# Performance work log

Measured on AMD Instinct MI355X. Metric: run time of the kernel, lower is better.

## Reference

```python
import jax, jax.numpy as jnp
import numpy as np

B, N_SRC, N_TGT = 2, 2048, 2048
DIM, HEADS, DIM_HEAD, DIM_ROT = 1024, 16, 64, 32
INNER = HEADS * DIM_HEAD
SCALE = DIM_HEAD ** -0.5


def rotate_every_two(x):
    # (..., d) with d even: pairs (x1, x2) -> (-x2, x1), interleaved
    x1 = x[..., ::2]
    x2 = x[..., 1::2]
    return jnp.stack((-x2, x1), axis=-1).reshape(x.shape)


def setup_inputs() -> dict:
    key = jax.random.key(0)
    ks = jax.random.split(key, 10)
    return {
        "src": jax.random.normal(ks[0], (B, N_SRC, DIM), jnp.float32),
        "sin_src": jax.random.uniform(ks[1], (B, N_SRC, DIM_ROT), jnp.float32, -1.0, 1.0),
        "cos_src": jax.random.uniform(ks[2], (B, N_SRC, DIM_ROT), jnp.float32, -1.0, 1.0),
        "tgt": jax.random.normal(ks[3], (B, N_TGT, DIM), jnp.float32),
        "sin_tgt": jax.random.uniform(ks[4], (B, N_TGT, DIM_ROT), jnp.float32, -1.0, 1.0),
        "cos_tgt": jax.random.uniform(ks[5], (B, N_TGT, DIM_ROT), jnp.float32, -1.0, 1.0),
        "wq": jax.random.normal(ks[6], (DIM, INNER), jnp.float32) / np.sqrt(DIM),
        "wkv": jax.random.normal(ks[7], (DIM, 2 * INNER), jnp.float32) / np.sqrt(DIM),
        "wout": jax.random.normal(ks[8], (INNER, DIM), jnp.float32) / np.sqrt(INNER),
        "bout": jnp.zeros((DIM,), jnp.float32),
    }


def reference(src, sin_src, cos_src, tgt, sin_tgt, cos_tgt, wq, wkv, wout, bout):
    b = src.shape[0]
    q = tgt @ wq                                  # (b, i, inner)
    k, v = jnp.split(src @ wkv, 2, axis=-1)       # (b, j, inner) each

    def split_heads(t):
        return t.reshape(b, t.shape[1], HEADS, DIM_HEAD).transpose(0, 2, 1, 3)

    q, k, v = map(split_heads, (q, k, v))          # (b, h, n, d)

    # rotary on leading DIM_ROT dims; pos embs broadcast across heads
    st, ct = sin_tgt[:, None], cos_tgt[:, None]    # (b, 1, i, dr)
    ss, cs = sin_src[:, None], cos_src[:, None]    # (b, 1, j, dr)
    q_rot, q_pass = q[..., :DIM_ROT], q[..., DIM_ROT:]
    k_rot, k_pass = k[..., :DIM_ROT], k[..., DIM_ROT:]
    q_rot = q_rot * ct + rotate_every_two(q_rot) * st
    k_rot = k_rot * cs + rotate_every_two(k_rot) * ss
    q = jnp.concatenate([q_rot, q_pass], axis=-1)
    k = jnp.concatenate([k_rot, k_pass], axis=-1)

    dots = jnp.einsum('bhid,bhjd->bhij', q, k) * SCALE
    attn = jax.nn.softmax(dots, axis=-1)
    out = jnp.einsum('bhij,bhjd->bhid', attn, v)
    out = out.transpose(0, 2, 1, 3).reshape(b, out.shape[2], INNER)
    return out @ wout + bout, attn
```

## Files before the change

kernel.cpp:

```cpp
#include <hip/hip_runtime.h>
#include <hip/hip_bf16.h>
#include <cstdint>
#include <cstddef>

#define NB 2
#define NSEQ 2048
#define NHEADS 16
#define HD 64
#define DMODEL 1024
#define SCALEF 0.125f

typedef __attribute__((ext_vector_type(4))) float f32x4;
typedef __attribute__((ext_vector_type(8))) short s16x8;

__device__ __forceinline__ unsigned short f2bf(float f) {
  union { float f; unsigned u; } v; v.f = f;
  unsigned u = v.u;
  return (unsigned short)((u + 0x7fffu + ((u >> 16) & 1u)) >> 16);
}
__device__ __forceinline__ float bf2f(unsigned short s) {
  union { unsigned u; float f; } v; v.u = ((unsigned)s) << 16;
  return v.f;
}

__global__ void k_convert(const float* __restrict__ in, unsigned short* __restrict__ out, int n4) {
  int i = blockIdx.x * blockDim.x + threadIdx.x;
  if (i >= n4) return;
  float4 v = ((const float4*)in)[i];
  ushort4 o;
  o.x = f2bf(v.x); o.y = f2bf(v.y); o.z = f2bf(v.z); o.w = f2bf(v.w);
  ((ushort4*)out)[i] = o;
}

__global__ void k_transpose(const float* __restrict__ w, unsigned short* __restrict__ wt, int K, int N) {
  __shared__ float t[64][65];
  int n0 = blockIdx.x * 64, k0 = blockIdx.y * 64;
  int c = threadIdx.x & 63, rb = threadIdx.x >> 6;
#pragma unroll
  for (int rr = 0; rr < 16; rr++) {
    int k = rb * 16 + rr;
    t[c][k] = w[(size_t)(k0 + k) * N + n0 + c];
  }
  __syncthreads();
#pragma unroll
  for (int rr = 0; rr < 16; rr++) {
    int n = rb * 16 + rr;
    wt[(size_t)(n0 + n) * K + k0 + c] = f2bf(t[n][c]);
  }
}

#define GLD16(gp, lp) __builtin_amdgcn_global_load_lds( \
    (const __attribute__((address_space(1))) unsigned int*)(gp), \
    (__attribute__((address_space(3))) unsigned int*)(lp), 16, 0, 0)

__global__ __launch_bounds__(256) void k_gemm(const unsigned short* __restrict__ A,
                                              const unsigned short* __restrict__ Bt,
                                              float* __restrict__ C,
                                              const float* __restrict__ bias,
                                              int M, int N, int K) {
  __shared__ unsigned short As[128 * 32];
  __shared__ unsigned short Bs[128 * 32];
  const int tid = threadIdx.x;
  const int lane = tid & 63, wid = tid >> 6;
  const int m0 = blockIdx.y * 128, n0 = blockIdx.x * 128;
  const int wr = wid >> 1, wc = wid & 1;
  const int lr = lane >> 2, l4 = lane & 3;
  const int lc = lane & 15, lg = lane >> 4;

  const unsigned short* pa0 = A + (size_t)(m0 + wid * 32 + lr) * K + l4 * 8;
  const unsigned short* pa1 = pa0 + (size_t)16 * K;
  const unsigned short* pb0 = Bt + (size_t)(n0 + wid * 32 + lr) * K + l4 * 8;
  const unsigned short* pb1 = pb0 + (size_t)16 * K;

  f32x4 acc[4][4] = {};

  for (int kt = 0; kt < K; kt += 32) {
    GLD16(pa0 + kt, &As[wid * 1024]);
    GLD16(pa1 + kt, &As[wid * 1024 + 512]);
    GLD16(pb0 + kt, &Bs[wid * 1024]);
    GLD16(pb1 + kt, &Bs[wid * 1024 + 512]);
    __syncthreads();
    s16x8 af[4], bfr[4];
#pragma unroll
    for (int m = 0; m < 4; m++)
      af[m] = *(const s16x8*)&As[(wr * 64 + m * 16 + lc) * 32 + lg * 8];
#pragma unroll
    for (int n = 0; n < 4; n++)
      bfr[n] = *(const s16x8*)&Bs[(wc * 64 + n * 16 + lc) * 32 + lg * 8];
    __builtin_amdgcn_s_setprio(1);
#pragma unroll
    for (int m = 0; m < 4; m++)
#pragma unroll
      for (int n = 0; n < 4; n++)
        acc[m][n] = __builtin_amdgcn_mfma_f32_16x16x32_bf16(af[m], bfr[n], acc[m][n], 0, 0, 0);
    __builtin_amdgcn_s_setprio(0);
    __syncthreads();
  }

  float bv[4] = {0.f, 0.f, 0.f, 0.f};
  if (bias) {
#pragma unroll
    for (int n = 0; n < 4; n++) bv[n] = bias[n0 + wc * 64 + n * 16 + lc];
  }
#pragma unroll
  for (int m = 0; m < 4; m++) {
#pragma unroll
    for (int n = 0; n < 4; n++) {
      int col = n0 + wc * 64 + n * 16 + lc;
#pragma unroll
      for (int r = 0; r < 4; r++) {
        int row = m0 + wr * 64 + m * 16 + lg * 4 + r;
        C[(size_t)row * N + col] = acc[m][n][r] + bv[n];
      }
    }
  }
}

__global__ void k_rope(const float* __restrict__ src, int row_stride,
                       const float* __restrict__ sinp, const float* __restrict__ cosp,
                       unsigned short* __restrict__ dst) {
  int tid = blockIdx.x * 256 + threadIdx.x;
  int p = tid & 31;
  int h = (tid >> 5) & 15;
  int i = (tid >> 9) & 2047;
  int b = tid >> 20;
  int d = p * 2;
  float2 x = *(const float2*)(src + (size_t)(b * NSEQ + i) * row_stride + h * HD + d);
  float o0, o1;
  if (p < 16) {
    size_t sc = (size_t)(b * NSEQ + i) * 32 + d;
    float2 cc = *(const float2*)(cosp + sc);
    float2 ss = *(const float2*)(sinp + sc);
    o0 = x.x * cc.x - x.y * ss.x;
    o1 = x.y * cc.y + x.x * ss.y;
  } else { o0 = x.x; o1 = x.y; }
  size_t off = ((size_t)(b * NHEADS + h) * NSEQ + i) * HD + d;
  unsigned pack = (unsigned)f2bf(o0) | ((unsigned)f2bf(o1) << 16);
  *(unsigned*)(dst + off) = pack;
}

__global__ void k_vtrans(const float* __restrict__ kv, unsigned short* __restrict__ vt) {
  __shared__ float t[64][65];
  int i0 = blockIdx.x * 64;
  int h = blockIdx.y, b = blockIdx.z;
  int c = threadIdx.x & 63, rb = threadIdx.x >> 6;
#pragma unroll
  for (int rr = 0; rr < 16; rr++) {
    int il = rb * 16 + rr;
    t[il][c] = kv[(size_t)(b * NSEQ + i0 + il) * 2048 + 1024 + h * HD + c];
  }
  __syncthreads();
#pragma unroll
  for (int rr = 0; rr < 16; rr++) {
    int dd = rb * 16 + rr;
    vt[((size_t)(b * NHEADS + h) * HD + dd) * NSEQ + i0 + c] = f2bf(t[c][dd]);
  }
}

#define QBLK 32
#define SROWB 2056
__global__ __launch_bounds__(1024, 4) void k_attn(const unsigned short* __restrict__ qh,
                                                  const unsigned short* __restrict__ kh,
                                                  const unsigned short* __restrict__ vt,
                                                  float* __restrict__ attn_g,
                                                  unsigned short* __restrict__ ctx) {
  __shared__ unsigned short Sbf[QBLK * SROWB];
  __shared__ float wred[16][32];
  __shared__ float invr[32];
  float* part = (float*)Sbf;

  const int tid = threadIdx.x;
  const int lane = tid & 63, wid = tid >> 6;
  const int i0 = blockIdx.x * QBLK;
  const int h = blockIdx.y, b = blockIdx.z;
  const int lc = lane & 15, lg = lane >> 4;
  const int wcb = wid * 128;

  const unsigned short* qb = qh + ((size_t)(b * NHEADS + h) * NSEQ + i0) * HD;
  const unsigned short* kb = kh + (size_t)(b * NHEADS + h) * NSEQ * HD;
  const unsigned short* vb = vt + (size_t)(b * NHEADS + h) * HD * NSEQ;

  s16x8 aq[2][2];
#pragma unroll
  for (int rg = 0; rg < 2; rg++) {
    aq[rg][0] = *(const s16x8*)&qb[(rg * 16 + lc) * HD + lg * 8];
    aq[rg][1] = *(const s16x8*)&qb[(rg * 16 + lc) * HD + 32 + lg * 8];
  }
  float psum[2][4] = {};
  const unsigned short* krow = kb + (size_t)(wcb + lc) * HD + lg * 8;
  s16x8 kp[2][2];
  kp[0][0] = *(const s16x8*)&krow[0];
  kp[0][1] = *(const s16x8*)&krow[32];
#pragma unroll
  for (int jf = 0; jf < 8; jf++) {
    if (jf < 7) {
      kp[(jf + 1) & 1][0] = *(const s16x8*)&krow[(size_t)((jf + 1) * 16) * HD];
      kp[(jf + 1) & 1][1] = *(const s16x8*)&krow[(size_t)((jf + 1) * 16) * HD + 32];
    }
    int j = wcb + jf * 16;
#pragma unroll
    for (int rg = 0; rg < 2; rg++) {
      f32x4 acc = {};
      acc = __builtin_amdgcn_mfma_f32_16x16x32_bf16(aq[rg][0], kp[jf & 1][0], acc, 0, 0, 0);
      acc = __builtin_amdgcn_mfma_f32_16x16x32_bf16(aq[rg][1], kp[jf & 1][1], acc, 0, 0, 0);
#pragma unroll
      for (int r = 0; r < 4; r++) {
        float e = __expf(acc[r] * SCALEF);
        psum[rg][r] += e;
        Sbf[(size_t)(rg * 16 + lg * 4 + r) * SROWB + j + lc] = f2bf(e);
      }
    }
  }
#pragma unroll
  for (int off = 1; off <= 8; off <<= 1)
#pragma unroll
    for (int rg = 0; rg < 2; rg++)
#pragma unroll
      for (int r = 0; r < 4; r++) psum[rg][r] += __shfl_xor(psum[rg][r], off);
  if (lc == 0) {
#pragma unroll
    for (int rg = 0; rg < 2; rg++)
#pragma unroll
      for (int r = 0; r < 4; r++) wred[wid][rg * 16 + lg * 4 + r] = psum[rg][r];
  }
  __syncthreads();
  if (tid < 32) {
    float tot = 0.f;
#pragma unroll
    for (int w = 0; w < 16; w++) tot += wred[w][tid];
    invr[tid] = 1.0f / tot;
  }

  f32x4 accd[2][4] = {};
  const unsigned short* vrow = vb + (size_t)lc * NSEQ + wcb + lg * 8;
  s16x8 vp[2][4];
#pragma unroll
  for (int f = 0; f < 4; f++)
    vp[0][f] = *(const s16x8*)&vrow[(size_t)(f * 16) * NSEQ];
#pragma unroll
  for (int jj = 0; jj < 4; jj++) {
    if (jj < 3) {
#pragma unroll
      for (int f = 0; f < 4; f++)
        vp[(jj + 1) & 1][f] = *(const s16x8*)&vrow[(size_t)(f * 16) * NSEQ + (jj + 1) * 32];
    }
    int jb = wcb + jj * 32;
    s16x8 af0 = *(const s16x8*)&Sbf[(size_t)lc * SROWB + jb + lg * 8];
    __builtin_amdgcn_s_setprio(1);
#pragma unroll
    for (int f = 0; f < 4; f++)
      accd[0][f] = __builtin_amdgcn_mfma_f32_16x16x32_bf16(af0, vp[jj & 1][f], accd[0][f], 0, 0, 0);
    __builtin_amdgcn_s_setprio(0);
    s16x8 af1 = *(const s16x8*)&Sbf[(size_t)(16 + lc) * SROWB + jb + lg * 8];
    __builtin_amdgcn_s_setprio(1);
#pragma unroll
    for (int f = 0; f < 4; f++)
      accd[1][f] = __builtin_amdgcn_mfma_f32_16x16x32_bf16(af1, vp[jj & 1][f], accd[1][f], 0, 0, 0);
    __builtin_amdgcn_s_setprio(0);
  }
  __syncthreads();

  {
    const int srow = tid >> 5;
    const int scc = (tid & 31) * 8;
    const float inv = invr[srow];
    float* arow = attn_g + ((size_t)(b * NHEADS + h) * NSEQ + i0 + srow) * NSEQ + scc;
#pragma unroll
    for (int k = 0; k < 8; k++) {
      s16x8 ev = *(const s16x8*)&Sbf[(size_t)srow * SROWB + scc + k * 256];
      f32x4 f0, f1;
      f0[0] = bf2f((unsigned short)ev[0]) * inv;
      f0[1] = bf2f((unsigned short)ev[1]) * inv;
      f0[2] = bf2f((unsigned short)ev[2]) * inv;
      f0[3] = bf2f((unsigned short)ev[3]) * inv;
      f1[0] = bf2f((unsigned short)ev[4]) * inv;
      f1[1] = bf2f((unsigned short)ev[5]) * inv;
      f1[2] = bf2f((unsigned short)ev[6]) * inv;
      f1[3] = bf2f((unsigned short)ev[7]) * inv;
      *(f32x4*)&arow[k * 256] = f0;
      *(f32x4*)&arow[k * 256 + 4] = f1;
    }
  }
  __syncthreads();

  if (wid < 8) {
#pragma unroll
    for (int rg = 0; rg < 2; rg++)
#pragma unroll
      for (int f = 0; f < 4; f++)
#pragma unroll
        for (int r = 0; r < 4; r++)
          part[((size_t)wid * 32 + rg * 16 + lg * 4 + r) * 64 + f * 16 + lc] = accd[rg][f][r];
  }
  __syncthreads();
  if (wid >= 8) {
#pragma unroll
    for (int rg = 0; rg < 2; rg++)
#pragma unroll
      for (int f = 0; f < 4; f++)
#pragma unroll
        for (int r = 0; r < 4; r++)
          part[((size_t)(wid - 8) * 32 + rg * 16 + lg * 4 + r) * 64 + f * 16 + lc] += accd[rg][f][r];
  }
  __syncthreads();

  {
    const int oi = tid >> 5;
    const int d0 = (tid & 31) * 2;
    float s0 = 0.f, s1 = 0.f;
#pragma unroll
    for (int p = 0; p < 8; p++) {
      s0 += part[((size_t)p * 32 + oi) * 64 + d0];
      s1 += part[((size_t)p * 32 + oi) * 64 + d0 + 1];
    }
    float iv = invr[oi];
    ushort2 o;
    o.x = f2bf(s0 * iv);
    o.y = f2bf(s1 * iv);
    *(ushort2*)&ctx[(size_t)(b * NSEQ + i0 + oi) * DMODEL + h * HD + d0] = o;
  }
}

extern "C" void kernel_launch(void* const* d_in, const int* in_sizes, int n_in,
                              void* d_out, int out_size, void* d_ws, size_t ws_size,
                              hipStream_t stream) {
  const float* src     = (const float*)d_in[0];
  const float* sin_src = (const float*)d_in[1];
  const float* cos_src = (const float*)d_in[2];
  const float* tgt     = (const float*)d_in[3];
  const float* sin_tgt = (const float*)d_in[4];
  const float* cos_tgt = (const float*)d_in[5];
  const float* wq      = (const float*)d_in[6];
  const float* wkv     = (const float*)d_in[7];
  const float* wout    = (const float*)d_in[8];
  const float* bout    = (const float*)d_in[9];

  if (ws_size < (size_t)109051904) return;

  uint8_t* w = (uint8_t*)d_ws;
  unsigned short* tgt_bf = (unsigned short*)(w + 0);
  unsigned short* src_bf = (unsigned short*)(w + 8388608);
  unsigned short* wq_t   = (unsigned short*)(w + 16777216);
  unsigned short* wkv_t  = (unsigned short*)(w + 18874368);
  unsigned short* wout_t = (unsigned short*)(w + 23068672);
  float*          q_ws   = (float*)(w + 25165824);
  float*          kv_ws  = (float*)(w + 41943040);
  unsigned short* qhb    = (unsigned short*)(w + 75497472);
  unsigned short* khb    = (unsigned short*)(w + 83886080);
  unsigned short* vtb    = (unsigned short*)(w + 92274688);
  unsigned short* ctx    = (unsigned short*)(w + 100663296);

  float* out_p  = (float*)d_out;
  float* attn_p = out_p + (size_t)NB * NSEQ * DMODEL;

  k_convert<<<4096, 256, 0, stream>>>(tgt, tgt_bf, 1048576);
  k_convert<<<4096, 256, 0, stream>>>(src, src_bf, 1048576);
  k_transpose<<<dim3(16, 16), 256, 0, stream>>>(wq,   wq_t,   1024, 1024);
  k_transpose<<<dim3(32, 16), 256, 0, stream>>>(wkv,  wkv_t,  1024, 2048);
  k_transpose<<<dim3(16, 16), 256, 0, stream>>>(wout, wout_t, 1024, 1024);

  k_gemm<<<dim3(8, 32),  256, 0, stream>>>(tgt_bf, wq_t,  q_ws,  nullptr, 4096, 1024, 1024);
  k_gemm<<<dim3(16, 32), 256, 0, stream>>>(src_bf, wkv_t, kv_ws, nullptr, 4096, 2048, 1024);

  k_rope<<<8192, 256, 0, stream>>>(q_ws, 1024, sin_tgt, cos_tgt, qhb);
  k_rope<<<8192, 256, 0, stream>>>(kv_ws, 2048, sin_src, cos_src, khb);
  k_vtrans<<<dim3(32, 16, 2), 256, 0, stream>>>(kv_ws, vtb);

  k_attn<<<dim3(64, 16, 2), 1024, 0, stream>>>(qhb, khb, vtb, attn_p, ctx);

  k_gemm<<<dim3(8, 32), 256, 0, stream>>>(ctx, wout_t, out_p, bout, 4096, 1024, 1024);
}
```

Baseline: 390.9 us.

## Keep softmax probabilities in registers, feeding PV MFMA directly without LDS staging

Swaps the QK^T MFMA operand order so each lane's accumulator holds a transposed score tile. The bf16 exponentials then stay in registers and serve directly as the B operand of a 16x16x16 MFMA for the PV product. This removes the 128KB LDS score buffer and its write/read traffic, and the attention-matrix writes are now issued straight from registers inside the PV loop. The V prefetch double-buffering is dropped, and inline asm MFMA with manual s_nop hazard padding adds correctness risk.

```diff
diff --git a/kernel.cpp b/kernel.cpp
--- a/kernel.cpp
+++ b/kernel.cpp
@@ -12,6 +12,7 @@
 
 typedef __attribute__((ext_vector_type(4))) float f32x4;
 typedef __attribute__((ext_vector_type(8))) short s16x8;
+typedef __attribute__((ext_vector_type(4))) short s16x4;
 
 __device__ __forceinline__ unsigned short f2bf(float f) {
   union { float f; unsigned u; } v; v.f = f;
@@ -158,16 +159,14 @@
 }
 
 #define QBLK 32
-#define SROWB 2056
 __global__ __launch_bounds__(1024, 4) void k_attn(const unsigned short* __restrict__ qh,
                                                   const unsigned short* __restrict__ kh,
                                                   const unsigned short* __restrict__ vt,
                                                   float* __restrict__ attn_g,
                                                   unsigned short* __restrict__ ctx) {
-  __shared__ unsigned short Sbf[QBLK * SROWB];
+  __shared__ float part[8][32][64];
   __shared__ float wred[16][32];
   __shared__ float invr[32];
-  float* part = (float*)Sbf;
 
   const int tid = threadIdx.x;
   const int lane = tid & 63, wid = tid >> 6;
@@ -182,46 +181,47 @@
 
   s16x8 aq[2][2];
 #pragma unroll
-  for (int rg = 0; rg < 2; rg++) {
-    aq[rg][0] = *(const s16x8*)&qb[(rg * 16 + lc) * HD + lg * 8];
-    aq[rg][1] = *(const s16x8*)&qb[(rg * 16 + lc) * HD + 32 + lg * 8];
-  }
-  float psum[2][4] = {};
+  for (int qg = 0; qg < 2; qg++) {
+    aq[qg][0] = *(const s16x8*)&qb[(qg * 16 + lc) * HD + lg * 8];
+    aq[qg][1] = *(const s16x8*)&qb[(qg * 16 + lc) * HD + 32 + lg * 8];
+  }
+
+  float psum[2] = {0.f, 0.f};
+  s16x4 ebf[2][8];
   const unsigned short* krow = kb + (size_t)(wcb + lc) * HD + lg * 8;
   s16x8 kp[2][2];
   kp[0][0] = *(const s16x8*)&krow[0];
   kp[0][1] = *(const s16x8*)&krow[32];
 #pragma unroll
-  for (int jf = 0; jf < 8; jf++) {
-    if (jf < 7) {
-      kp[(jf + 1) & 1][0] = *(const s16x8*)&krow[(size_t)((jf + 1) * 16) * HD];
-      kp[(jf + 1) & 1][1] = *(const s16x8*)&krow[(size_t)((jf + 1) * 16) * HD + 32];
-    }
-    int j = wcb + jf * 16;
-#pragma unroll
-    for (int rg = 0; rg < 2; rg++) {
+  for (int jt = 0; jt < 8; jt++) {
+    if (jt < 7) {
+      kp[(jt + 1) & 1][0] = *(const s16x8*)&krow[(size_t)((jt + 1) * 16) * HD];
+      kp[(jt + 1) & 1][1] = *(const s16x8*)&krow[(size_t)((jt + 1) * 16) * HD + 32];
+    }
+#pragma unroll
+    for (int qg = 0; qg < 2; qg++) {
       f32x4 acc = {};
-      acc = __builtin_amdgcn_mfma_f32_16x16x32_bf16(aq[rg][0], kp[jf & 1][0], acc, 0, 0, 0);
-      acc = __builtin_amdgcn_mfma_f32_16x16x32_bf16(aq[rg][1], kp[jf & 1][1], acc, 0, 0, 0);
-#pragma unroll
-      for (int r = 0; r < 4; r++) {
-        float e = __expf(acc[r] * SCALEF);
-        psum[rg][r] += e;
-        Sbf[(size_t)(rg * 16 + lg * 4 + r) * SROWB + j + lc] = f2bf(e);
-      }
-    }
-  }
-#pragma unroll
-  for (int off = 1; off <= 8; off <<= 1)
-#pragma unroll
-    for (int rg = 0; rg < 2; rg++)
-#pragma unroll
-      for (int r = 0; r < 4; r++) psum[rg][r] += __shfl_xor(psum[rg][r], off);
-  if (lc == 0) {
-#pragma unroll
-    for (int rg = 0; rg < 2; rg++)
-#pragma unroll
-      for (int r = 0; r < 4; r++) wred[wid][rg * 16 + lg * 4 + r] = psum[rg][r];
+      acc = __builtin_amdgcn_mfma_f32_16x16x32_bf16(kp[jt & 1][0], aq[qg][0], acc, 0, 0, 0);
+      acc = __builtin_amdgcn_mfma_f32_16x16x32_bf16(kp[jt & 1][1], aq[qg][1], acc, 0, 0, 0);
+      float e0 = __expf(acc[0] * SCALEF);
+      float e1 = __expf(acc[1] * SCALEF);
+      float e2 = __expf(acc[2] * SCALEF);
+      float e3 = __expf(acc[3] * SCALEF);
+      psum[qg] += (e0 + e1) + (e2 + e3);
+      s16x4 p;
+      p[0] = (short)f2bf(e0); p[1] = (short)f2bf(e1);
+      p[2] = (short)f2bf(e2); p[3] = (short)f2bf(e3);
+      ebf[qg][jt] = p;
+    }
+  }
+#pragma unroll
+  for (int qg = 0; qg < 2; qg++) {
+    psum[qg] += __shfl_xor(psum[qg], 16);
+    psum[qg] += __shfl_xor(psum[qg], 32);
+  }
+  if (lg == 0) {
+    wred[wid][lc] = psum[0];
+    wred[wid][16 + lc] = psum[1];
   }
   __syncthreads();
   if (tid < 32) {
@@ -230,77 +230,59 @@
     for (int w = 0; w < 16; w++) tot += wred[w][tid];
     invr[tid] = 1.0f / tot;
   }
-
-  f32x4 accd[2][4] = {};
-  const unsigned short* vrow = vb + (size_t)lc * NSEQ + wcb + lg * 8;
-  s16x8 vp[2][4];
-#pragma unroll
-  for (int f = 0; f < 4; f++)
-    vp[0][f] = *(const s16x8*)&vrow[(size_t)(f * 16) * NSEQ];
-#pragma unroll
-  for (int jj = 0; jj < 4; jj++) {
-    if (jj < 3) {
-#pragma unroll
-      for (int f = 0; f < 4; f++)
-        vp[(jj + 1) & 1][f] = *(const s16x8*)&vrow[(size_t)(f * 16) * NSEQ + (jj + 1) * 32];
-    }
-    int jb = wcb + jj * 32;
-    s16x8 af0 = *(const s16x8*)&Sbf[(size_t)lc * SROWB + jb + lg * 8];
-    __builtin_amdgcn_s_setprio(1);
-#pragma unroll
-    for (int f = 0; f < 4; f++)
-      accd[0][f] = __builtin_amdgcn_mfma_f32_16x16x32_bf16(af0, vp[jj & 1][f], accd[0][f], 0, 0, 0);
-    __builtin_amdgcn_s_setprio(0);
-    s16x8 af1 = *(const s16x8*)&Sbf[(size_t)(16 + lc) * SROWB + jb + lg * 8];
-    __builtin_amdgcn_s_setprio(1);
-#pragma unroll
-    for (int f = 0; f < 4; f++)
-      accd[1][f] = __builtin_amdgcn_mfma_f32_16x16x32_bf16(af1, vp[jj & 1][f], accd[1][f], 0, 0, 0);
-    __builtin_amdgcn_s_setprio(0);
-  }
-  __syncthreads();
-
-  {
-    const int srow = tid >> 5;
-    const int scc = (tid & 31) * 8;
-    const float inv = invr[srow];
-    float* arow = attn_g + ((size_t)(b * NHEADS + h) * NSEQ + i0 + srow) * NSEQ + scc;
-#pragma unroll
-    for (int k = 0; k < 8; k++) {
-      s16x8 ev = *(const s16x8*)&Sbf[(size_t)srow * SROWB + scc + k * 256];
-      f32x4 f0, f1;
-      f0[0] = bf2f((unsigned short)ev[0]) * inv;
-      f0[1] = bf2f((unsigned short)ev[1]) * inv;
-      f0[2] = bf2f((unsigned short)ev[2]) * inv;
-      f0[3] = bf2f((unsigned short)ev[3]) * inv;
-      f1[0] = bf2f((unsigned short)ev[4]) * inv;
-      f1[1] = bf2f((unsigned short)ev[5]) * inv;
-      f1[2] = bf2f((unsigned short)ev[6]) * inv;
-      f1[3] = bf2f((unsigned short)ev[7]) * inv;
-      *(f32x4*)&arow[k * 256] = f0;
-      *(f32x4*)&arow[k * 256 + 4] = f1;
-    }
-  }
-  __syncthreads();
+  __syncthreads();
+  const float inv0 = invr[lc];
+  const float inv1 = invr[16 + lc];
+
+  f32x4 acc_o[4][2] = {};
+  float* arow0 = attn_g + ((size_t)(b * NHEADS + h) * NSEQ + i0 + lc) * NSEQ + wcb + lg * 4;
+  float* arow1 = arow0 + (size_t)16 * NSEQ;
+#pragma unroll
+  for (int jt = 0; jt < 8; jt++) {
+    s16x4 vf[4];
+#pragma unroll
+    for (int dt = 0; dt < 4; dt++)
+      vf[dt] = *(const s16x4*)&vb[(size_t)(dt * 16 + lc) * NSEQ + wcb + jt * 16 + lg * 4];
+    {
+      f32x4 s0, s1;
+#pragma unroll
+      for (int r = 0; r < 4; r++) {
+        s0[r] = bf2f((unsigned short)ebf[0][jt][r]) * inv0;
+        s1[r] = bf2f((unsigned short)ebf[1][jt][r]) * inv1;
+      }
+      *(f32x4*)&arow0[jt * 16] = s0;
+      *(f32x4*)&arow1[jt * 16] = s1;
+    }
+#pragma unroll
+    for (int dt = 0; dt < 4; dt++) {
+#pragma unroll
+      for (int qg = 0; qg < 2; qg++) {
+        asm volatile("v_mfma_f32_16x16x16_bf16 %0, %1, %2, %0"
+                     : "+v"(acc_o[dt][qg])
+                     : "v"(vf[dt]), "v"(ebf[qg][jt]));
+      }
+    }
+  }
+  asm volatile("s_nop 7\n\ts_nop 7" ::: "memory");
 
   if (wid < 8) {
 #pragma unroll
-    for (int rg = 0; rg < 2; rg++)
-#pragma unroll
-      for (int f = 0; f < 4; f++)
+    for (int dt = 0; dt < 4; dt++)
+#pragma unroll
+      for (int qg = 0; qg < 2; qg++)
 #pragma unroll
         for (int r = 0; r < 4; r++)
-          part[((size_t)wid * 32 + rg * 16 + lg * 4 + r) * 64 + f * 16 + lc] = accd[rg][f][r];
+          part[wid][qg * 16 + lc][dt * 16 + lg * 4 + r] = acc_o[dt][qg][r];
   }
   __syncthreads();
   if (wid >= 8) {
 #pragma unroll
-    for (int rg = 0; rg < 2; rg++)
-#pragma unroll
-      for (int f = 0; f < 4; f++)
+    for (int dt = 0; dt < 4; dt++)
+#pragma unroll
+      for (int qg = 0; qg < 2; qg++)
 #pragma unroll
         for (int r = 0; r < 4; r++)
-          part[((size_t)(wid - 8) * 32 + rg * 16 + lg * 4 + r) * 64 + f * 16 + lc] += accd[rg][f][r];
+          part[wid - 8][qg * 16 + lc][dt * 16 + lg * 4 + r] += acc_o[dt][qg][r];
   }
   __syncthreads();
 
@@ -310,8 +292,8 @@
     float s0 = 0.f, s1 = 0.f;
 #pragma unroll
     for (int p = 0; p < 8; p++) {
-      s0 += part[((size_t)p * 32 + oi) * 64 + d0];
-      s1 += part[((size_t)p * 32 + oi) * 64 + d0 + 1];
+      s0 += part[p][oi][d0];
+      s1 += part[p][oi][d0 + 1];
     }
     float iv = invr[oi];
     ushort2 o;
```

Measured after the change: 473.2 us. +21.1%, slower.
